# Kernel tuning notes

Measured on AMD Instinct MI355X. Metric: run time of the kernel, lower is better.

## Reference

```python
import jax, jax.numpy as jnp
import numpy as np


def setup_inputs() -> dict:
    key = jax.random.key(0)
    B, D, C, H = 4096, 64, 128, 512
    ks = jax.random.split(key, 6)
    return {
        "q_z_x_params": jax.random.normal(ks[0], (B, C), jnp.float32),
        "eps": jax.random.normal(ks[1], (B, D), jnp.float32),
        "W1": jax.random.normal(ks[2], (D + C, H), jnp.float32) / np.sqrt(D + C).astype(np.float32),
        "b1": jnp.zeros((H,), jnp.float32),
        "W2": jax.random.normal(ks[3], (H, H), jnp.float32) / np.sqrt(H).astype(np.float32),
        "b2": jnp.zeros((H,), jnp.float32),
        "W3": jax.random.normal(ks[4], (H, 2 * D), jnp.float32) / np.sqrt(H).astype(np.float32),
        "b3": jnp.zeros((2 * D,), jnp.float32),
    }


def _made_masks(D, C, H):
    # Standard MADE degrees, natural ordering; context columns fully connected.
    m_in = np.arange(1, D + 1)                      # input degrees 1..D
    m_h = (np.arange(H) % (D - 1)) + 1              # hidden degrees 1..D-1
    M1 = np.concatenate([m_h[None, :] >= m_in[:, None],
                         np.ones((C, H), bool)], axis=0)   # (D+C, H)
    M2 = m_h[None, :] >= m_h[:, None]               # (H, H)
    m_out = np.tile(np.arange(1, D + 1), 2)         # (2D,) mean||prescale
    M3 = m_out[None, :] > m_h[:, None]              # (H, 2D)
    f32 = jnp.float32
    return jnp.asarray(M1, f32), jnp.asarray(M2, f32), jnp.asarray(M3, f32)


def reference(q_z_x_params, eps, W1, b1, W2, b2, W3, b3):
    B, D = eps.shape
    C = q_z_x_params.shape[1]
    H = W2.shape[0]
    M1, M2, M3 = _made_masks(D, C, H)
    mW1, mW2, mW3 = W1 * M1, W2 * M2, W3 * M3

    def made(z):
        x = jnp.concatenate([z, q_z_x_params], axis=1)   # (B, D+C)
        h1 = jax.nn.relu(x @ mW1 + b1)
        h2 = jax.nn.relu(h1 @ mW2 + b2)
        out = h2 @ mW3 + b3                              # (B, 2D)
        return out[:, :D], out[:, D:]

    def step(z, i):
        mean, prescale = made(z)
        mu_i = jnp.take(mean, i, axis=1)                 # (B,)
        scale_i = jax.nn.softplus(jnp.take(prescale, i, axis=1))
        z_i = mu_i + scale_i * jnp.take(eps, i, axis=1)  # reparameterized Normal sample
        z = z.at[:, i].set(z_i)
        return z, None

    z0 = jnp.zeros((B, D), eps.dtype)
    z_sample, _ = jax.lax.scan(step, z0, jnp.arange(D))
    return z_sample
```

## Files before the change

kernel.cpp:

```cpp
#include <hip/hip_runtime.h>
#include <math.h>

#define DD 64
#define CC 128
#define HH 512
#define BATCH 4096

typedef __attribute__((ext_vector_type(2))) float f32x2;

__device__ __forceinline__ f32x2 splat2(float x) { f32x2 v; v[0] = x; v[1] = x; return v; }

__device__ __forceinline__ float fast_softplus(float x) {
    float t = exp2f(-fabsf(x) * 1.44269504f);
    return fmaxf(x, 0.f) + 0.69314718f * log2f(1.f + t);
}

__device__ __forceinline__ float bcast(float x, int l) {
    return __int_as_float(__builtin_amdgcn_readlane(__float_as_int(x), l));
}

typedef const __attribute__((address_space(1))) void* as1_cptr;
typedef __attribute__((address_space(3))) void* as3_ptr;
__device__ __forceinline__ void glds16(const float* g, float* l) {
    __builtin_amdgcn_global_load_lds((as1_cptr)g, (as3_ptr)l, 16, 0, 0);
}

__global__ __launch_bounds__(256, 2) void made_sample(
    const float* __restrict__ ctx,
    const float* __restrict__ eps,
    const float* __restrict__ W1,
    const float* __restrict__ b1,
    const float* __restrict__ W2,
    const float* __restrict__ b2,
    const float* __restrict__ W3,
    const float* __restrict__ b3,
    float* __restrict__ out)
{
    const int lane  = threadIdx.x & 63;
    const int w     = threadIdx.x >> 6;
    const int rbase = blockIdx.x * 8 + w * 2;
    const int jbase = 8 * lane;

    __shared__ float sbuf[2][10 * HH];

    int deg[8];
    #pragma unroll
    for (int u = 0; u < 8; ++u) deg[u] = (jbase + u) % 63 + 1;

    auto load8v = [&](const float* base_, f32x2* r_) {
        float4 a = *(const float4*)(base_ + lane * 4);
        float4 b = *(const float4*)(base_ + 256 + lane * 4);
        r_[0][0] = a.x; r_[0][1] = a.y; r_[1][0] = a.z; r_[1][1] = a.w;
        r_[2][0] = b.x; r_[2][1] = b.y; r_[3][0] = b.z; r_[3][1] = b.w;
    };
    auto stage_row = [&](const float* src, float* dst) {
        glds16(src + lane * 8,     dst);
        glds16(src + lane * 8 + 4, dst + 256);
    };

    f32x2 p1[2][4], p2[2][4], acc[2];
    #pragma unroll
    for (int j = 0; j < 4; ++j) {
        f32x2 t1, t2;
        t1[0] = b1[jbase + 2 * j]; t1[1] = b1[jbase + 2 * j + 1];
        t2[0] = b2[jbase + 2 * j]; t2[1] = b2[jbase + 2 * j + 1];
        p1[0][j] = t1; p1[1][j] = t1;
        p2[0][j] = t2; p2[1][j] = t2;
    }
    acc[0] = splat2(0.f);
    acc[1] = splat2(0.f);

    float ca[2], cb[2], ep[2];
    #pragma unroll
    for (int r = 0; r < 2; ++r) {
        ca[r] = ctx[(rbase + r) * CC + lane];
        cb[r] = ctx[(rbase + r) * CC + 64 + lane];
        ep[r] = eps[(rbase + r) * DD + lane];
    }
    const float b3m = b3[lane];
    const float b3p = b3[64 + lane];

    auto stage_ctx = [&](int ch, float* buf) {
        #pragma unroll
        for (int q2 = 0; q2 < 2; ++q2) {
            const int q = 2 * w + q2;
            stage_row(W1 + (DD + 8 * ch + q) * HH, buf + q * HH);
        }
    };
    auto stage_step = [&](int in, float* buf) {
        const int basen = (in == 0) ? 0 : (in - 1);
        #pragma unroll
        for (int rr = 0; rr < 3; ++rr) {
            const int r = w + 4 * rr;
            if (r <= 9) {
                const float* src;
                if (r < 9) {
                    int k = basen + 63 * r;
                    if (k >= HH) k = HH - 8;
                    src = W2 + k * HH;
                } else {
                    src = W1 + in * HH;
                }
                stage_row(src, buf + r * HH);
            }
        }
    };

    stage_ctx(0, sbuf[0]);
    __syncthreads();
    #pragma unroll 1
    for (int ch = 0; ch < 16; ++ch) {
        float* cur = sbuf[ch & 1];
        float* nxt = sbuf[(ch + 1) & 1];
        if (ch < 15) stage_ctx(ch + 1, nxt);
        else         stage_step(0, sbuf[0]);
        #pragma unroll
        for (int q = 0; q < 8; ++q) {
            f32x2 wv[4];
            load8v(cur + q * HH, wv);
            const int c = 8 * ch + q;
            #pragma unroll
            for (int r = 0; r < 2; ++r) {
                const float cv = bcast((ch < 8) ? ca[r] : cb[r], c & 63);
                const f32x2 cv2 = splat2(cv);
                #pragma unroll
                for (int j = 0; j < 4; ++j) p1[r][j] += cv2 * wv[j];
            }
        }
        __syncthreads();
    }

    float z[2] = {0.f, 0.f};

    #pragma unroll 1
    for (int i = 0; i < DD; ++i) {
        float* cur = sbuf[i & 1];
        float* nxt = sbuf[(i + 1) & 1];
        if (i < 63) stage_step(i + 1, nxt);

        const int base = (i == 0) ? 0 : (i - 1);

        f32x2 w3v[9];
        #pragma unroll
        for (int t = 0; t < 9; ++t) {
            const int k  = base + 63 * t;
            const int ks = (k < HH) ? k : (HH - 1);
            w3v[t][0] = W3[ks * (2 * DD) + lane];
            w3v[t][1] = W3[ks * (2 * DD) + 64 + lane];
        }

        float m[2];
        #pragma unroll
        for (int r = 0; r < 2; ++r) {
            float mv = 0.f;
            #pragma unroll
            for (int u = 0; u < 8; ++u)
                mv = (deg[u] == i) ? p1[r][u >> 1][u & 1] : mv;
            m[r] = fmaxf(mv, 0.f);
        }

        #pragma unroll
        for (int t = 0; t < 9; ++t) {
            const int k = base + 63 * t;
            f32x2 wv[4];
            load8v(cur + t * HH, wv);
            float h0, h1v;
            if (t == 8) {
                const float vm = (k < HH) ? 1.f : 0.f;
                h0  = vm * bcast(m[0], 63);
                h1v = vm * bcast(m[1], 63);
            } else {
                h0  = bcast(m[0], k >> 3);
                h1v = bcast(m[1], k >> 3);
            }
            const f32x2 h0v = splat2(h0), h1vv = splat2(h1v);
            #pragma unroll
            for (int j = 0; j < 4; ++j) {
                p2[0][j] += h0v  * wv[j];
                p2[1][j] += h1vv * wv[j];
            }
        }

        float hn[2];
        #pragma unroll
        for (int r = 0; r < 2; ++r) {
            float hv = 0.f;
            #pragma unroll
            for (int u = 0; u < 8; ++u)
                hv = (deg[u] == i) ? p2[r][u >> 1][u & 1] : hv;
            hn[r] = fmaxf(hv, 0.f);
        }

        #pragma unroll
        for (int t = 0; t < 9; ++t) {
            const int k = base + 63 * t;
            float h0, h1v;
            if (t == 8) {
                const float vm = (k < HH) ? 1.f : 0.f;
                h0  = vm * bcast(hn[0], 63);
                h1v = vm * bcast(hn[1], 63);
            } else {
                h0  = bcast(hn[0], k >> 3);
                h1v = bcast(hn[1], k >> 3);
            }
            acc[0] += splat2(h0)  * w3v[t];
            acc[1] += splat2(h1v) * w3v[t];
        }

        f32x2 w1v[4];
        load8v(cur + 9 * HH, w1v);
        #pragma unroll
        for (int r = 0; r < 2; ++r) {
            const float am = acc[r][0] + b3m;
            const float ap = acc[r][1] + b3p;
            const float sp = fast_softplus(ap);
            const float zc = fmaf(sp, ep[r], am);
            const float zi = bcast(zc, i);
            if (lane == i) z[r] = zi;
            const f32x2 zi2 = splat2(zi);
            #pragma unroll
            for (int j = 0; j < 4; ++j) p1[r][j] += zi2 * w1v[j];
        }

        __syncthreads();
    }

    #pragma unroll
    for (int r = 0; r < 2; ++r) out[(rbase + r) * DD + lane] = z[r];
}

extern "C" void kernel_launch(void* const* d_in, const int* in_sizes, int n_in,
                              void* d_out, int out_size, void* d_ws, size_t ws_size,
                              hipStream_t stream) {
    const float* ctx = (const float*)d_in[0];
    const float* eps = (const float*)d_in[1];
    const float* W1  = (const float*)d_in[2];
    const float* b1  = (const float*)d_in[3];
    const float* W2  = (const float*)d_in[4];
    const float* b2  = (const float*)d_in[5];
    const float* W3  = (const float*)d_in[6];
    const float* b3  = (const float*)d_in[7];
    (void)d_ws; (void)ws_size; (void)in_sizes; (void)n_in; (void)out_size;

    made_sample<<<BATCH / 8, 256, 0, stream>>>(ctx, eps, W1, b1, W2, b2, W3, b3,
                                               (float*)d_out);
}
```

Measured before the change: 187.3 us.

## Stage W3 rows into LDS asynchronously, skip step zero work, force packed FMA

W3 rows needed per autoregressive step are now prefetched into a double-buffered LDS area with global_load_lds alongside the W2/W1 rows, replacing per-step global loads that sat on the critical path. Step 0 skips the hidden-layer updates entirely, and the ninth W2/W3 term is only loaded and applied when its index is in range, instead of being masked by multiplication. The inner accumulations use inline v_pk_fma_f32 asm so the packed FMA is guaranteed. The costs are extra LDS per block and inline asm that may constrain compiler scheduling.

```diff
diff --git a/kernel.cpp b/kernel.cpp
--- a/kernel.cpp
+++ b/kernel.cpp
@@ -9,6 +9,12 @@
 typedef __attribute__((ext_vector_type(2))) float f32x2;
 
 __device__ __forceinline__ f32x2 splat2(float x) { f32x2 v; v[0] = x; v[1] = x; return v; }
+
+__device__ __forceinline__ f32x2 pk_fma(f32x2 a, f32x2 b, f32x2 c) {
+    f32x2 d;
+    asm("v_pk_fma_f32 %0, %1, %2, %3" : "=v"(d) : "v"(a), "v"(b), "v"(c));
+    return d;
+}
 
 __device__ __forceinline__ float fast_softplus(float x) {
     float t = exp2f(-fabsf(x) * 1.44269504f);
@@ -42,6 +48,7 @@
     const int jbase = 8 * lane;
 
     __shared__ float sbuf[2][10 * HH];
+    __shared__ float w3sb[2][5 * 256];
 
     int deg[8];
     #pragma unroll
@@ -56,6 +63,11 @@
     auto stage_row = [&](const float* src, float* dst) {
         glds16(src + lane * 8,     dst);
         glds16(src + lane * 8 + 4, dst + 256);
+    };
+    auto stage_w3pair = [&](int k0, int k1, float* dst) {
+        const float* g = (lane < 32) ? (W3 + k0 * (2 * DD) + lane * 4)
+                                     : (W3 + k1 * (2 * DD) + (lane - 32) * 4);
+        glds16(g, dst);
     };
 
     f32x2 p1[2][4], p2[2][4], acc[2];
@@ -87,21 +99,26 @@
             stage_row(W1 + (DD + 8 * ch + q) * HH, buf + q * HH);
         }
     };
-    auto stage_step = [&](int in, float* buf) {
-        const int basen = (in == 0) ? 0 : (in - 1);
-        #pragma unroll
-        for (int rr = 0; rr < 3; ++rr) {
-            const int r = w + 4 * rr;
-            if (r <= 9) {
-                const float* src;
-                if (r < 9) {
-                    int k = basen + 63 * r;
-                    if (k >= HH) k = HH - 8;
-                    src = W2 + k * HH;
-                } else {
-                    src = W1 + in * HH;
-                }
-                stage_row(src, buf + r * HH);
+    auto stage_step = [&](int in, float* buf, float* w3buf) {
+        if (in == 0) {
+            if (w == 1) stage_row(W1, buf + 9 * HH);
+            return;
+        }
+        const int basen = in - 1;
+        const bool h9n = basen < 8;
+        stage_row(W2 + (basen + 63 * w) * HH,       buf + w * HH);
+        stage_row(W2 + (basen + 63 * (4 + w)) * HH, buf + (4 + w) * HH);
+        if (w == 1) stage_row(W1 + in * HH, buf + 9 * HH);
+        if (w == 0 && h9n) {
+            stage_row(W2 + (basen + 504) * HH, buf + 8 * HH);
+            stage_w3pair(basen + 504, basen + 504, w3buf + 4 * 256);
+        }
+        if (w >= 2) {
+            #pragma unroll
+            for (int pp = 0; pp < 2; ++pp) {
+                const int p = 2 * (w - 2) + pp;
+                stage_w3pair(basen + 63 * (2 * p), basen + 63 * (2 * p + 1),
+                             w3buf + p * 256);
             }
         }
     };
@@ -113,7 +130,7 @@
         float* cur = sbuf[ch & 1];
         float* nxt = sbuf[(ch + 1) & 1];
         if (ch < 15) stage_ctx(ch + 1, nxt);
-        else         stage_step(0, sbuf[0]);
+        else         stage_step(0, sbuf[0], w3sb[0]);
         #pragma unroll
         for (int q = 0; q < 8; ++q) {
             f32x2 wv[4];
@@ -124,7 +141,7 @@
                 const float cv = bcast((ch < 8) ? ca[r] : cb[r], c & 63);
                 const f32x2 cv2 = splat2(cv);
                 #pragma unroll
-                for (int j = 0; j < 4; ++j) p1[r][j] += cv2 * wv[j];
+                for (int j = 0; j < 4; ++j) p1[r][j] = pk_fma(cv2, wv[j], p1[r][j]);
             }
         }
         __syncthreads();
@@ -135,91 +152,97 @@
     #pragma unroll 1
     for (int i = 0; i < DD; ++i) {
         float* cur = sbuf[i & 1];
-        float* nxt = sbuf[(i + 1) & 1];
-        if (i < 63) stage_step(i + 1, nxt);
-
-        const int base = (i == 0) ? 0 : (i - 1);
-
-        f32x2 w3v[9];
-        #pragma unroll
-        for (int t = 0; t < 9; ++t) {
-            const int k  = base + 63 * t;
-            const int ks = (k < HH) ? k : (HH - 1);
-            w3v[t][0] = W3[ks * (2 * DD) + lane];
-            w3v[t][1] = W3[ks * (2 * DD) + 64 + lane];
-        }
-
-        float m[2];
-        #pragma unroll
-        for (int r = 0; r < 2; ++r) {
-            float mv = 0.f;
-            #pragma unroll
-            for (int u = 0; u < 8; ++u)
-                mv = (deg[u] == i) ? p1[r][u >> 1][u & 1] : mv;
-            m[r] = fmaxf(mv, 0.f);
-        }
-
-        #pragma unroll
-        for (int t = 0; t < 9; ++t) {
-            const int k = base + 63 * t;
-            f32x2 wv[4];
-            load8v(cur + t * HH, wv);
-            float h0, h1v;
-            if (t == 8) {
-                const float vm = (k < HH) ? 1.f : 0.f;
-                h0  = vm * bcast(m[0], 63);
-                h1v = vm * bcast(m[1], 63);
-            } else {
-                h0  = bcast(m[0], k >> 3);
-                h1v = bcast(m[1], k >> 3);
-            }
-            const f32x2 h0v = splat2(h0), h1vv = splat2(h1v);
-            #pragma unroll
-            for (int j = 0; j < 4; ++j) {
-                p2[0][j] += h0v  * wv[j];
-                p2[1][j] += h1vv * wv[j];
-            }
-        }
-
-        float hn[2];
-        #pragma unroll
-        for (int r = 0; r < 2; ++r) {
-            float hv = 0.f;
-            #pragma unroll
-            for (int u = 0; u < 8; ++u)
-                hv = (deg[u] == i) ? p2[r][u >> 1][u & 1] : hv;
-            hn[r] = fmaxf(hv, 0.f);
-        }
-
-        #pragma unroll
-        for (int t = 0; t < 9; ++t) {
-            const int k = base + 63 * t;
-            float h0, h1v;
-            if (t == 8) {
-                const float vm = (k < HH) ? 1.f : 0.f;
-                h0  = vm * bcast(hn[0], 63);
-                h1v = vm * bcast(hn[1], 63);
-            } else {
-                h0  = bcast(hn[0], k >> 3);
-                h1v = bcast(hn[1], k >> 3);
-            }
-            acc[0] += splat2(h0)  * w3v[t];
-            acc[1] += splat2(h1v) * w3v[t];
-        }
-
-        f32x2 w1v[4];
-        load8v(cur + 9 * HH, w1v);
-        #pragma unroll
-        for (int r = 0; r < 2; ++r) {
-            const float am = acc[r][0] + b3m;
-            const float ap = acc[r][1] + b3p;
-            const float sp = fast_softplus(ap);
-            const float zc = fmaf(sp, ep[r], am);
-            const float zi = bcast(zc, i);
-            if (lane == i) z[r] = zi;
-            const f32x2 zi2 = splat2(zi);
-            #pragma unroll
-            for (int j = 0; j < 4; ++j) p1[r][j] += zi2 * w1v[j];
+        const float* w3s = w3sb[i & 1];
+        if (i < 63) stage_step(i + 1, sbuf[(i + 1) & 1], w3sb[(i + 1) & 1]);
+
+        if (i > 0) {
+            const int base = i - 1;
+            const bool h9 = base < 8;
+
+            float m0 = 0.f, m1 = 0.f;
+            #pragma unroll
+            for (int u = 0; u < 8; ++u) {
+                const bool e = (deg[u] == i);
+                m0 = e ? p1[0][u >> 1][u & 1] : m0;
+                m1 = e ? p1[1][u >> 1][u & 1] : m1;
+            }
+            m0 = fmaxf(m0, 0.f);
+            m1 = fmaxf(m1, 0.f);
+
+            #pragma unroll
+            for (int t = 0; t < 8; ++t) {
+                const int k = base + 63 * t;
+                f32x2 wv[4];
+                load8v(cur + t * HH, wv);
+                const f32x2 h0 = splat2(bcast(m0, k >> 3));
+                const f32x2 h1 = splat2(bcast(m1, k >> 3));
+                #pragma unroll
+                for (int j = 0; j < 4; ++j) {
+                    p2[0][j] = pk_fma(h0, wv[j], p2[0][j]);
+                    p2[1][j] = pk_fma(h1, wv[j], p2[1][j]);
+                }
+            }
+            if (h9) {
+                f32x2 wv[4];
+                load8v(cur + 8 * HH, wv);
+                const f32x2 h0 = splat2(bcast(m0, 63));
+                const f32x2 h1 = splat2(bcast(m1, 63));
+                #pragma unroll
+                for (int j = 0; j < 4; ++j) {
+                    p2[0][j] = pk_fma(h0, wv[j], p2[0][j]);
+                    p2[1][j] = pk_fma(h1, wv[j], p2[1][j]);
+                }
+            }
+
+            float g0 = 0.f, g1 = 0.f;
+            #pragma unroll
+            for (int u = 0; u < 8; ++u) {
+                const bool e = (deg[u] == i);
+                g0 = e ? p2[0][u >> 1][u & 1] : g0;
+                g1 = e ? p2[1][u >> 1][u & 1] : g1;
+            }
+            g0 = fmaxf(g0, 0.f);
+            g1 = fmaxf(g1, 0.f);
+
+            #pragma unroll
+            for (int t = 0; t < 8; ++t) {
+                const int k = base + 63 * t;
+                const float wa = w3s[t * 128 + lane];
+                const float wb = w3s[t * 128 + 64 + lane];
+                const float h0 = bcast(g0, k >> 3);
+                const float h1 = bcast(g1, k >> 3);
+                acc[0][0] = fmaf(h0, wa, acc[0][0]);
+                acc[0][1] = fmaf(h0, wb, acc[0][1]);
+                acc[1][0] = fmaf(h1, wa, acc[1][0]);
+                acc[1][1] = fmaf(h1, wb, acc[1][1]);
+            }
+            if (h9) {
+                const float wa = w3s[8 * 128 + lane];
+                const float wb = w3s[8 * 128 + 64 + lane];
+                const float h0 = bcast(g0, 63);
+                const float h1 = bcast(g1, 63);
+                acc[0][0] = fmaf(h0, wa, acc[0][0]);
+                acc[0][1] = fmaf(h0, wb, acc[0][1]);
+                acc[1][0] = fmaf(h1, wa, acc[1][0]);
+                acc[1][1] = fmaf(h1, wb, acc[1][1]);
+            }
+        }
+
+        {
+            f32x2 w1v[4];
+            load8v(cur + 9 * HH, w1v);
+            #pragma unroll
+            for (int r = 0; r < 2; ++r) {
+                const float am = acc[r][0] + b3m;
+                const float ap = acc[r][1] + b3p;
+                const float sp = fast_softplus(ap);
+                const float zc = fmaf(sp, ep[r], am);
+                const float zi = bcast(zc, i);
+                if (lane == i) z[r] = zi;
+                const f32x2 zi2 = splat2(zi);
+                #pragma unroll
+                for (int j = 0; j < 4; ++j) p1[r][j] = pk_fma(zi2, w1v[j], p1[r][j]);
+            }
         }
 
         __syncthreads();
```

Measured after the change: 178.8 us. 1.05x faster.
